# Performance work log

Measured on AMD Instinct MI355X. Metric: run time of the kernel, lower is better.

The kernel has to match this reference:

```python
import jax, jax.numpy as jnp
import numpy as np

B, S, HID = 1, 2048, 2048
H, KH, D = 16, 8, 128          # query heads, kv heads, head_dim
GROUPS = H // KH                # num_key_value_groups = 2
EPS = 1e-6
SCALE = D ** -0.5
NEG = -1e9


def rmsnorm(x, w):
    # torch.nn.RMSNorm over last dim with learned weight
    return x * jax.lax.rsqrt(jnp.mean(x * x, axis=-1, keepdims=True) + EPS) * w


def rope(x, cos, sin):
    # x: [b, s, h, d]; cos/sin: [s, d//2]  (rotate-half style, matching apply_rotary_emb_single)
    half = x.shape[-1] // 2
    xr, xi = x[..., :half], x[..., half:]
    c = cos[None, :, None, :]
    s = sin[None, :, None, :]
    return jnp.concatenate([xr * c - xi * s, xr * s + xi * c], axis=-1)


def setup_inputs() -> dict:
    key = jax.random.key(0)
    ks = jax.random.split(key, 8)
    hidden_states = jax.random.normal(ks[0], (B, S, HID), jnp.float32)
    # real RoPE angle tables (theta=1e6, Qwen3-style), shape [S, D//2]
    inv_freq = 1.0 / (1e6 ** (np.arange(0, D, 2, dtype=np.float32) / D))
    ang = np.arange(S, dtype=np.float32)[:, None] * inv_freq[None, :]
    freqs_cos = jnp.asarray(np.cos(ang), jnp.float32)
    freqs_sin = jnp.asarray(np.sin(ang), jnp.float32)
    # additive causal mask [1, S, S]
    causal = jnp.tril(jnp.ones((S, S), jnp.bool_))
    atten_mask = jnp.where(causal, 0.0, NEG).astype(jnp.float32)[None]
    # learned params (no bias: attention_bias=False)
    Wq = jax.random.normal(ks[1], (H * D, HID), jnp.float32) * 0.02
    Wk = jax.random.normal(ks[2], (KH * D, HID), jnp.float32) * 0.02
    Wv = jax.random.normal(ks[3], (KH * D, HID), jnp.float32) * 0.02
    Wo = jax.random.normal(ks[4], (HID, H * D), jnp.float32) * 0.02
    q_norm_w = 1.0 + 0.01 * jax.random.normal(ks[5], (D,), jnp.float32)
    k_norm_w = 1.0 + 0.01 * jax.random.normal(ks[6], (D,), jnp.float32)
    return {"hidden_states": hidden_states, "freqs_cos": freqs_cos, "freqs_sin": freqs_sin,
            "atten_mask": atten_mask, "Wq": Wq, "Wk": Wk, "Wv": Wv, "Wo": Wo,
            "q_norm_w": q_norm_w, "k_norm_w": k_norm_w}


def reference(hidden_states, freqs_cos, freqs_sin, atten_mask, Wq, Wk, Wv, Wo, q_norm_w, k_norm_w):
    b, s, _ = hidden_states.shape
    q = (hidden_states @ Wq.T).reshape(b, s, H, D)
    k = (hidden_states @ Wk.T).reshape(b, s, KH, D)
    v = (hidden_states @ Wv.T).reshape(b, s, KH, D)
    q = rope(rmsnorm(q, q_norm_w), freqs_cos, freqs_sin)
    k = rope(rmsnorm(k, k_norm_w), freqs_cos, freqs_sin)
    # GQA: head i uses kv head i // GROUPS -> repeat kv heads in-order
    k_exp = jnp.repeat(k, GROUPS, axis=2)  # [b, s, H, d]
    v_exp = jnp.repeat(v, GROUPS, axis=2)
    scores = jnp.einsum('bshd,bthd->bhst', q, k_exp) * SCALE + atten_mask[:, None, :, :]
    attn = jax.nn.softmax(scores, axis=-1)
    y = jnp.einsum('bhst,bthd->bshd', attn, v_exp).reshape(b, s, H * D)
    y = y @ Wo.T
    # output_new_cache_only: last-position k (post-norm/RoPE) and raw v per kv head
    k_new = jnp.transpose(k[:, -1], (1, 0, 2))  # [KH, b, D]
    v_new = jnp.transpose(v[:, -1], (1, 0, 2))  # [KH, b, D]
    return y, k_new, v_new
```

## Files before the change

### kernel.cpp

```cpp
#include <hip/hip_runtime.h>
#include <hip/hip_bf16.h>
#include <math.h>

#define S_LEN 2048
#define HID 2048
#define NH 16
#define NKH 8
#define HD 128
#define QKV_N 4096
#define SCALE 0.08838834764831845f
#define EPS 1e-6f
#define LOG2E 1.4426950408889634f
#define QSCALE (SCALE * LOG2E)

typedef __hip_bfloat16 bf16;
typedef unsigned int u32;
typedef __bf16 bf16x8 __attribute__((ext_vector_type(8)));
typedef float f32x4 __attribute__((ext_vector_type(4)));

#define MFMA(a, b, c) __builtin_amdgcn_mfma_f32_16x16x32_bf16(a, b, c, 0, 0, 0)

static __device__ __forceinline__ bf16x8 ld_frag(const bf16* p) {
    return __builtin_bit_cast(bf16x8, *(const uint4*)p);
}

static __device__ __forceinline__ void gload_lds16(const void* g, void* l) {
    __builtin_amdgcn_global_load_lds(
        (const __attribute__((address_space(1))) u32*)g,
        (__attribute__((address_space(3))) u32*)l, 16, 0, 0);
}

__global__ __launch_bounds__(256) void cvt5(
    const float* __restrict__ s0, const float* __restrict__ s1,
    const float* __restrict__ s2, const float* __restrict__ s3,
    const float* __restrict__ s4,
    bf16* __restrict__ d0, bf16* __restrict__ d1, bf16* __restrict__ d2,
    bf16* __restrict__ d3, bf16* __restrict__ d4)
{
    int i = blockIdx.x * 256 + threadIdx.x;
    const float* s; bf16* d; int off;
    if (i < (1 << 20))                   { s = s0; d = d0; off = 0; }
    else if (i < (2 << 20))              { s = s1; d = d1; off = 1 << 20; }
    else if (i < (2 << 20) + (1 << 19))  { s = s2; d = d2; off = 2 << 20; }
    else if (i < (3 << 20))              { s = s3; d = d3; off = (2 << 20) + (1 << 19); }
    else                                 { s = s4; d = d4; off = 3 << 20; }
    int j = i - off;
    float4 v = ((const float4*)s)[j];
    union { ushort4 u; bf16 h[4]; } o;
    o.h[0] = __float2bfloat16(v.x);
    o.h[1] = __float2bfloat16(v.y);
    o.h[2] = __float2bfloat16(v.z);
    o.h[3] = __float2bfloat16(v.w);
    *(ushort4*)(d + 4 * (size_t)j) = o.u;
}

__global__ __launch_bounds__(256, 2) void gemm_qkv(
    const bf16* __restrict__ A, const bf16* __restrict__ B,
    bf16* __restrict__ qkvb, bf16* __restrict__ vT,
    const float* __restrict__ fcos, const float* __restrict__ fsin,
    const float* __restrict__ qw, const float* __restrict__ kw,
    float* __restrict__ knew, float* __restrict__ vnew)
{
    __shared__ bf16 As[2][128 * 64];
    __shared__ bf16 Bs[2][128 * 64];
    __shared__ float red[2][2][64];
    const int tid = threadIdx.x;
    const int n0 = blockIdx.x * 128, m0 = blockIdx.y * 128;
    const int w = tid >> 6, lane = tid & 63;
    const int l15 = lane & 15, quad = lane >> 4;
    const int wr = (w >> 1) * 64;
    const int wcg = (w & 1) * 32;

    f32x4 acc[4][4];
    #pragma unroll
    for (int i = 0; i < 4; ++i)
        #pragma unroll
        for (int j = 0; j < 4; ++j)
            acc[i][j] = f32x4{0.f, 0.f, 0.f, 0.f};

    const int srow8 = lane >> 3;
    const int sls = ((lane & 7) ^ srow8) * 8;

    auto stage = [&](int k0, int nb) {
        #pragma unroll
        for (int j = 0; j < 8; ++j) {
            int c = 8 * w + j;
            if (c < 16) {
                int row = c * 8 + srow8;
                gload_lds16(A + (size_t)(m0 + row) * HID + k0 + sls, &As[nb][c * 512]);
            } else {
                int row = (c - 16) * 8 + srow8;
                gload_lds16(B + (size_t)(n0 + row) * HID + k0 + sls, &Bs[nb][(c - 16) * 512]);
            }
        }
    };

    stage(0, 0);
    for (int kt = 0; kt < HID / 64; ++kt) {
        const int pp = kt & 1;
        __syncthreads();
        if (kt + 1 < HID / 64) stage((kt + 1) * 64, pp ^ 1);

        #pragma unroll
        for (int kc = 0; kc < 2; ++kc) {
            const int ph = ((kc * 4 + quad) ^ (l15 & 7)) * 8;
            bf16x8 av[4], bv[4];
            #pragma unroll
            for (int i = 0; i < 4; ++i)
                av[i] = ld_frag(&As[pp][(wr + i * 16 + l15) * 64 + ph]);
            #pragma unroll
            for (int j = 0; j < 4; ++j)
                bv[j] = ld_frag(&Bs[pp][(wcg + (j & 1) * 16 + (j >> 1) * 64 + l15) * 64 + ph]);
            #pragma unroll
            for (int i = 0; i < 4; ++i)
                #pragma unroll
                for (int j = 0; j < 4; ++j)
                    acc[i][j] = MFMA(av[i], bv[j], acc[i][j]);
        }
    }

    const int hblk = n0 >> 7;
    if (hblk < 24) {
        float ssq[4][4];
        #pragma unroll
        for (int i = 0; i < 4; ++i)
            #pragma unroll
            for (int rr = 0; rr < 4; ++rr) {
                float ss = 0.f;
                #pragma unroll
                for (int j = 0; j < 4; ++j) ss += acc[i][j][rr] * acc[i][j][rr];
                ss += __shfl_xor(ss, 1);
                ss += __shfl_xor(ss, 2);
                ss += __shfl_xor(ss, 4);
                ss += __shfl_xor(ss, 8);
                ssq[i][rr] = ss;
                if (l15 == 0)
                    red[w >> 1][w & 1][i * 16 + quad * 4 + rr] = ss;
            }
        __syncthreads();

        const float* wgt = (hblk < 16) ? qw : kw;
        float wv[4];
        #pragma unroll
        for (int j = 0; j < 4; ++j)
            wv[j] = wgt[wcg + (j & 1) * 16 + (j >> 1) * 64 + l15];
        const size_t cb = (hblk < 16) ? (size_t)hblk * HD
                                      : (size_t)HID + (size_t)(hblk - 16) * HD;

        #pragma unroll
        for (int i = 0; i < 4; ++i)
            #pragma unroll
            for (int rr = 0; rr < 4; ++rr) {
                int rloc = i * 16 + quad * 4 + rr;
                int srow = m0 + wr + rloc;
                float tot = ssq[i][rr] + red[w >> 1][(w & 1) ^ 1][rloc];
                float rrn = rsqrtf(tot * (1.0f / 128.0f) + EPS);
                float x[4], res[4];
                #pragma unroll
                for (int j = 0; j < 4; ++j) x[j] = acc[i][j][rr] * rrn * wv[j];
                #pragma unroll
                for (int j2 = 0; j2 < 2; ++j2) {
                    float c = fcos[srow * 64 + wcg + j2 * 16 + l15];
                    float s = fsin[srow * 64 + wcg + j2 * 16 + l15];
                    res[j2]     = x[j2] * c - x[j2 + 2] * s;
                    res[j2 + 2] = x[j2] * s + x[j2 + 2] * c;
                }
                if (hblk < 16) {
                    #pragma unroll
                    for (int j = 0; j < 4; ++j)
                        qkvb[(size_t)srow * QKV_N + cb + wcg + (j & 1) * 16 +
                             (j >> 1) * 64 + l15] = __float2bfloat16(res[j] * QSCALE);
                } else {
                    #pragma unroll
                    for (int j = 0; j < 4; ++j)
                        qkvb[(size_t)srow * QKV_N + cb + wcg + (j & 1) * 16 +
                             (j >> 1) * 64 + l15] = __float2bfloat16(res[j]);
                    if (srow == S_LEN - 1) {
                        #pragma unroll
                        for (int j = 0; j < 4; ++j)
                            knew[(hblk - 16) * HD + wcg + (j & 1) * 16 +
                                 (j >> 1) * 64 + l15] = res[j];
                    }
                }
            }
    } else {
        const int kh = hblk - 24;
        #pragma unroll
        for (int i = 0; i < 4; ++i) {
            int rowbase = m0 + wr + i * 16 + quad * 4;
            #pragma unroll
            for (int j = 0; j < 4; ++j) {
                int d = wcg + (j & 1) * 16 + (j >> 1) * 64 + l15;
                union { uint2 u; bf16 hh[4]; } pk;
                #pragma unroll
                for (int r = 0; r < 4; ++r)
                    pk.hh[r] = __float2bfloat16(acc[i][j][r]);
                *(uint2*)&vT[(size_t)(kh * HD + d) * S_LEN + rowbase] = pk.u;
                if (rowbase == S_LEN - 4)
                    vnew[kh * HD + d] = acc[i][j][3];
            }
        }
    }
}

__global__ __launch_bounds__(256, 2) void gemm_n64(
    const bf16* __restrict__ A, const bf16* __restrict__ B,
    float* __restrict__ C, int M, int N, int K)
{
    __shared__ bf16 As[2][128 * 64];
    __shared__ bf16 Bs[2][64 * 64];
    const int tid = threadIdx.x;
    const int n0 = blockIdx.x * 64, m0 = blockIdx.y * 128;
    const int w = tid >> 6, lane = tid & 63;
    const int l15 = lane & 15, quad = lane >> 4;

    f32x4 acc[2][4];
    #pragma unroll
    for (int i = 0; i < 2; ++i)
        #pragma unroll
        for (int j = 0; j < 4; ++j)
            acc[i][j] = f32x4{0.f, 0.f, 0.f, 0.f};

    const int srow8 = lane >> 3;
    const int sls = ((lane & 7) ^ srow8) * 8;

    auto stage = [&](int k0, int nb) {
        #pragma unroll
        for (int j = 0; j < 6; ++j) {
            int c = 6 * w + j;
            if (c < 16) {
                int row = c * 8 + srow8;
                gload_lds16(A + (size_t)(m0 + row) * K + k0 + sls, &As[nb][c * 512]);
            } else {
                int row = (c - 16) * 8 + srow8;
                gload_lds16(B + (size_t)(n0 + row) * K + k0 + sls, &Bs[nb][(c - 16) * 512]);
            }
        }
    };

    stage(0, 0);
    for (int kt = 0; kt < K / 64; ++kt) {
        const int pp = kt & 1;
        __syncthreads();
        if (kt + 1 < K / 64) stage((kt + 1) * 64, pp ^ 1);

        #pragma unroll
        for (int kc = 0; kc < 2; ++kc) {
            const int ph = ((kc * 4 + quad) ^ (l15 & 7)) * 8;
            bf16x8 av[2], bv[4];
            av[0] = ld_frag(&As[pp][(w * 32 + l15) * 64 + ph]);
            av[1] = ld_frag(&As[pp][(w * 32 + 16 + l15) * 64 + ph]);
            #pragma unroll
            for (int j = 0; j < 4; ++j)
                bv[j] = ld_frag(&Bs[pp][(j * 16 + l15) * 64 + ph]);
            #pragma unroll
            for (int i = 0; i < 2; ++i)
                #pragma unroll
                for (int j = 0; j < 4; ++j)
                    acc[i][j] = MFMA(av[i], bv[j], acc[i][j]);
        }
    }

    #pragma unroll
    for (int i = 0; i < 2; ++i)
        #pragma unroll
        for (int j = 0; j < 4; ++j)
            #pragma unroll
            for (int r = 0; r < 4; ++r)
                C[(size_t)(m0 + w * 32 + i * 16 + quad * 4 + r) * N +
                  n0 + j * 16 + l15] = acc[i][j][r];
}

__global__ __launch_bounds__(256, 2) void attn_mfma(
    const bf16* __restrict__ qkvb, const bf16* __restrict__ vT,
    bf16* __restrict__ outb)
{
    __shared__ bf16 Ks[2][64 * 128];
    __shared__ bf16 Vs[2][128 * 64];
    __shared__ bf16 Ps[4][16 * 72];
    __shared__ float lred[4][4][16];

    const int x = blockIdx.x;
    const int h = blockIdx.y, kvh = h >> 1;
    int a = (x & 1) ? (31 - (x >> 1)) : (x >> 1);
    const int qb = (h < 8) ? a : 31 - a;
    const int tid = threadIdx.x, w = tid >> 6, lane = tid & 63;
    const int l15 = lane & 15, quad = lane >> 4;

    bf16x8 qf[4][4];
    #pragma unroll
    for (int j = 0; j < 4; ++j)
        #pragma unroll
        for (int dk = 0; dk < 4; ++dk)
            qf[j][dk] = ld_frag(qkvb + (size_t)(qb * 64 + j * 16 + l15) * QKV_N +
                                h * HD + dk * 32 + quad * 8);

    f32x4 o[8];
    #pragma unroll
    for (int dt = 0; dt < 8; ++dt) o[dt] = f32x4{0.f, 0.f, 0.f, 0.f};
    float l_st[4] = {0.f, 0.f, 0.f, 0.f};

    auto stage = [&](int t, int nb) {
        const int kt0 = t * 64;
        if (w < 2) {
            #pragma unroll
            for (int c = 0; c < 8; ++c) {
                int chunk = w * 8 + c;
                int row = 4 * chunk + (lane >> 4);
                int ls = (lane & 15) ^ (row & 15);
                gload_lds16(qkvb + (size_t)(kt0 + row) * QKV_N + HID +
                            kvh * HD + ls * 8,
                            &Ks[nb][chunk * 512]);
            }
        } else {
            #pragma unroll
            for (int c = 0; c < 8; ++c) {
                int chunk = (w - 2) * 8 + c;
                int row = 8 * chunk + (lane >> 3);
                int ls = (lane & 7) ^ ((lane >> 3) & 7);
                gload_lds16(vT + (size_t)(kvh * HD + row) * S_LEN + kt0 + ls * 8,
                            &Vs[nb][chunk * 512]);
            }
        }
    };

    stage(0, 0);
    for (int t = 0; t <= qb; ++t) {
        const int pp = t & 1;
        __syncthreads();
        if (t < qb) stage(t + 1, pp ^ 1);

        f32x4 sc[4];
        #pragma unroll
        for (int j = 0; j < 4; ++j) sc[j] = f32x4{0.f, 0.f, 0.f, 0.f};
        #pragma unroll
        for (int dk = 0; dk < 4; ++dk) {
            bf16x8 kf = ld_frag(&Ks[pp][(w * 16 + l15) * 128 +
                                        (((dk * 4 + quad) ^ l15) & 15) * 8]);
            #pragma unroll
            for (int j = 0; j < 4; ++j)
                sc[j] = MFMA(kf, qf[j][dk], sc[j]);
        }

        if (t == qb) {
            #pragma unroll
            for (int j = 0; j < 4; ++j)
                #pragma unroll
                for (int r = 0; r < 4; ++r)
                    if (w * 16 + quad * 4 + r > j * 16 + l15) sc[j][r] = -1e30f;
        }

        #pragma unroll
        for (int j = 0; j < 4; ++j) {
            union { uint2 u; bf16 hh[4]; } pk;
            #pragma unroll
            for (int r = 0; r < 4; ++r) {
                float p = exp2f(sc[j][r]);
                pk.hh[r] = __float2bfloat16(p);
                l_st[j] += p;
            }
            *(uint2*)&Ps[j][l15 * 72 + w * 16 + quad * 4] = pk.u;
        }

        asm volatile("s_waitcnt lgkmcnt(0)" ::: "memory");
        __builtin_amdgcn_s_barrier();

        #pragma unroll
        for (int kc = 0; kc < 2; ++kc) {
            bf16x8 pf[4];
            #pragma unroll
            for (int j = 0; j < 4; ++j)
                pf[j] = ld_frag(&Ps[j][l15 * 72 + kc * 32 + quad * 8]);
            #pragma unroll
            for (int dt = 0; dt < 2; ++dt) {
                bf16x8 vf = ld_frag(&Vs[pp][((w * 2 + dt) * 16 + l15) * 64 +
                                            (((kc * 4 + quad) ^ (l15 & 7)) * 8)]);
                #pragma unroll
                for (int j = 0; j < 4; ++j)
                    o[dt * 4 + j] = MFMA(vf, pf[j], o[dt * 4 + j]);
            }
        }
    }

    #pragma unroll
    for (int j = 0; j < 4; ++j) {
        l_st[j] += __shfl_xor(l_st[j], 16, 64);
        l_st[j] += __shfl_xor(l_st[j], 32, 64);
    }
    if (lane < 16) {
        #pragma unroll
        for (int j = 0; j < 4; ++j) lred[w][j][lane] = l_st[j];
    }
    __syncthreads();
    #pragma unroll
    for (int j = 0; j < 4; ++j) {
        float inv = 1.0f / (lred[0][j][l15] + lred[1][j][l15] +
                            lred[2][j][l15] + lred[3][j][l15]);
        int qg = qb * 64 + j * 16 + l15;
        #pragma unroll
        for (int dt = 0; dt < 2; ++dt) {
            union { uint2 u; bf16 hh[4]; } pk;
            #pragma unroll
            for (int r = 0; r < 4; ++r)
                pk.hh[r] = __float2bfloat16(o[dt * 4 + j][r] * inv);
            *(uint2*)&outb[(size_t)qg * HID + h * HD + w * 32 + dt * 16 + quad * 4] = pk.u;
        }
    }
}

extern "C" void kernel_launch(void* const* d_in, const int* in_sizes, int n_in,
                              void* d_out, int out_size, void* d_ws, size_t ws_size,
                              hipStream_t stream) {
    const float* hidden = (const float*)d_in[0];
    const float* fcos   = (const float*)d_in[1];
    const float* fsin   = (const float*)d_in[2];
    const float* Wq = (const float*)d_in[4];
    const float* Wk = (const float*)d_in[5];
    const float* Wv = (const float*)d_in[6];
    const float* Wo = (const float*)d_in[7];
    const float* qw = (const float*)d_in[8];
    const float* kw = (const float*)d_in[9];
    float* out = (float*)d_out;

    bf16* qkvb  = (bf16*)d_ws;
    bf16* vT    = qkvb + (size_t)S_LEN * QKV_N;
    bf16* attnb = vT + (size_t)NKH * HD * S_LEN;
    bf16* wqkvb = attnb + (size_t)S_LEN * HID;
    bf16* hidb  = wqkvb + (size_t)QKV_N * HID;
    bf16* wob   = hidb + (size_t)S_LEN * HID;

    float* knew = out + (size_t)S_LEN * HID;
    float* vnew = knew + NKH * HD;

    cvt5<<<16384, 256, 0, stream>>>(
        hidden, Wq, Wk, Wv, Wo,
        hidb, wqkvb, wqkvb + (size_t)HID * HID,
        wqkvb + (size_t)(HID + NKH * HD) * HID, wob);

    gemm_qkv<<<dim3(QKV_N / 128, S_LEN / 128), 256, 0, stream>>>(
        hidb, wqkvb, qkvb, vT, fcos, fsin, qw, kw, knew, vnew);

    attn_mfma<<<dim3(32, NH), 256, 0, stream>>>(qkvb, vT, attnb);

    gemm_n64<<<dim3(HID / 64, S_LEN / 128), 256, 0, stream>>>(
        attnb, wob, out, S_LEN, HID, HID);
}
```

Before: 240.6 us.

## Fuse fp32-to-bf16 conversion into GEMM operand staging, drop separate convert kernel

Removes the standalone conversion kernel that turned hidden states and all weights into bf16 in workspace. The QKV and output-projection GEMMs now load fp32 operands into registers, convert them to bf16 and write them to LDS, software-pipelined one tile ahead. This drops a full read/write pass over the inputs and weights and one launch. In exchange the GEMMs move twice the bytes per tile from global/L2 and use more registers in place of direct global-to-LDS loads.

```diff
diff --git a/kernel.cpp b/kernel.cpp
--- a/kernel.cpp
+++ b/kernel.cpp
@@ -30,32 +30,20 @@
         (__attribute__((address_space(3))) u32*)l, 16, 0, 0);
 }
 
-__global__ __launch_bounds__(256) void cvt5(
-    const float* __restrict__ s0, const float* __restrict__ s1,
-    const float* __restrict__ s2, const float* __restrict__ s3,
-    const float* __restrict__ s4,
-    bf16* __restrict__ d0, bf16* __restrict__ d1, bf16* __restrict__ d2,
-    bf16* __restrict__ d3, bf16* __restrict__ d4)
-{
-    int i = blockIdx.x * 256 + threadIdx.x;
-    const float* s; bf16* d; int off;
-    if (i < (1 << 20))                   { s = s0; d = d0; off = 0; }
-    else if (i < (2 << 20))              { s = s1; d = d1; off = 1 << 20; }
-    else if (i < (2 << 20) + (1 << 19))  { s = s2; d = d2; off = 2 << 20; }
-    else if (i < (3 << 20))              { s = s3; d = d3; off = (2 << 20) + (1 << 19); }
-    else                                 { s = s4; d = d4; off = 3 << 20; }
-    int j = i - off;
-    float4 v = ((const float4*)s)[j];
-    union { ushort4 u; bf16 h[4]; } o;
-    o.h[0] = __float2bfloat16(v.x);
-    o.h[1] = __float2bfloat16(v.y);
-    o.h[2] = __float2bfloat16(v.z);
-    o.h[3] = __float2bfloat16(v.w);
-    *(ushort4*)(d + 4 * (size_t)j) = o.u;
+static __device__ __forceinline__ uint4 cvt8(float4 lo, float4 hi) {
+    union { uint4 u; bf16 h[8]; } pk;
+    pk.h[0] = __float2bfloat16(lo.x); pk.h[1] = __float2bfloat16(lo.y);
+    pk.h[2] = __float2bfloat16(lo.z); pk.h[3] = __float2bfloat16(lo.w);
+    pk.h[4] = __float2bfloat16(hi.x); pk.h[5] = __float2bfloat16(hi.y);
+    pk.h[6] = __float2bfloat16(hi.z); pk.h[7] = __float2bfloat16(hi.w);
+    return pk.u;
 }
 
 __global__ __launch_bounds__(256, 2) void gemm_qkv(
-    const bf16* __restrict__ A, const bf16* __restrict__ B,
+    const float* __restrict__ A,
+    const float* __restrict__ Wq,
+    const float* __restrict__ Wk,
+    const float* __restrict__ Wv,
     bf16* __restrict__ qkvb, bf16* __restrict__ vT,
     const float* __restrict__ fcos, const float* __restrict__ fsin,
     const float* __restrict__ qw, const float* __restrict__ kw,
@@ -71,6 +59,12 @@
     const int wr = (w >> 1) * 64;
     const int wcg = (w & 1) * 32;
 
+    const int hblk = n0 >> 7;
+    const float* Bsrc; int brow0;
+    if (hblk < 16)      { Bsrc = Wq; brow0 = n0; }
+    else if (hblk < 24) { Bsrc = Wk; brow0 = n0 - 2048; }
+    else                { Bsrc = Wv; brow0 = n0 - 3072; }
+
     f32x4 acc[4][4];
     #pragma unroll
     for (int i = 0; i < 4; ++i)
@@ -81,25 +75,36 @@
     const int srow8 = lane >> 3;
     const int sls = ((lane & 7) ^ srow8) * 8;
 
-    auto stage = [&](int k0, int nb) {
+    float4 rlo[8], rhi[8];
+
+    auto issue = [&](int k0) {
         #pragma unroll
         for (int j = 0; j < 8; ++j) {
             int c = 8 * w + j;
-            if (c < 16) {
-                int row = c * 8 + srow8;
-                gload_lds16(A + (size_t)(m0 + row) * HID + k0 + sls, &As[nb][c * 512]);
-            } else {
-                int row = (c - 16) * 8 + srow8;
-                gload_lds16(B + (size_t)(n0 + row) * HID + k0 + sls, &Bs[nb][(c - 16) * 512]);
-            }
-        }
-    };
-
-    stage(0, 0);
+            const float* src = (c < 16)
+                ? A    + (size_t)(m0 + c * 8 + srow8) * HID + k0 + sls
+                : Bsrc + (size_t)(brow0 + (c - 16) * 8 + srow8) * HID + k0 + sls;
+            rlo[j] = *(const float4*)src;
+            rhi[j] = *(const float4*)(src + 4);
+        }
+    };
+    auto writeb = [&](int nb) {
+        #pragma unroll
+        for (int j = 0; j < 8; ++j) {
+            int c = 8 * w + j;
+            uint4 u = cvt8(rlo[j], rhi[j]);
+            bf16* dst = (c < 16)
+                ? &As[nb][c * 512 + srow8 * 64 + (lane & 7) * 8]
+                : &Bs[nb][(c - 16) * 512 + srow8 * 64 + (lane & 7) * 8];
+            *(uint4*)dst = u;
+        }
+    };
+
+    issue(0);  writeb(0);
+    issue(64);
     for (int kt = 0; kt < HID / 64; ++kt) {
         const int pp = kt & 1;
         __syncthreads();
-        if (kt + 1 < HID / 64) stage((kt + 1) * 64, pp ^ 1);
 
         #pragma unroll
         for (int kc = 0; kc < 2; ++kc) {
@@ -117,9 +122,13 @@
                 for (int j = 0; j < 4; ++j)
                     acc[i][j] = MFMA(av[i], bv[j], acc[i][j]);
         }
-    }
-
-    const int hblk = n0 >> 7;
+
+        if (kt + 1 < HID / 64) {
+            writeb(pp ^ 1);
+            if (kt + 2 < HID / 64) issue((kt + 2) * 64);
+        }
+    }
+
     if (hblk < 24) {
         float ssq[4][4];
         #pragma unroll
@@ -204,7 +213,7 @@
 }
 
 __global__ __launch_bounds__(256, 2) void gemm_n64(
-    const bf16* __restrict__ A, const bf16* __restrict__ B,
+    const bf16* __restrict__ A, const float* __restrict__ Bw,
     float* __restrict__ C, int M, int N, int K)
 {
     __shared__ bf16 As[2][128 * 64];
@@ -224,25 +233,38 @@
     const int srow8 = lane >> 3;
     const int sls = ((lane & 7) ^ srow8) * 8;
 
-    auto stage = [&](int k0, int nb) {
-        #pragma unroll
-        for (int j = 0; j < 6; ++j) {
-            int c = 6 * w + j;
-            if (c < 16) {
-                int row = c * 8 + srow8;
-                gload_lds16(A + (size_t)(m0 + row) * K + k0 + sls, &As[nb][c * 512]);
-            } else {
-                int row = (c - 16) * 8 + srow8;
-                gload_lds16(B + (size_t)(n0 + row) * K + k0 + sls, &Bs[nb][(c - 16) * 512]);
-            }
-        }
-    };
-
-    stage(0, 0);
+    auto stageA = [&](int k0, int nb) {
+        #pragma unroll
+        for (int j = 0; j < 4; ++j) {
+            int c = 4 * w + j;
+            gload_lds16(A + (size_t)(m0 + c * 8 + srow8) * K + k0 + sls,
+                        &As[nb][c * 512]);
+        }
+    };
+    float4 blo[2], bhi[2];
+    auto issueB = [&](int k0) {
+        #pragma unroll
+        for (int j = 0; j < 2; ++j) {
+            const float* src = Bw + (size_t)(n0 + (2 * w + j) * 8 + srow8) * K + k0 + sls;
+            blo[j] = *(const float4*)src;
+            bhi[j] = *(const float4*)(src + 4);
+        }
+    };
+    auto writeB = [&](int nb) {
+        #pragma unroll
+        for (int j = 0; j < 2; ++j) {
+            uint4 u = cvt8(blo[j], bhi[j]);
+            *(uint4*)&Bs[nb][(2 * w + j) * 512 + srow8 * 64 + (lane & 7) * 8] = u;
+        }
+    };
+
+    issueB(0);  writeB(0);
+    stageA(0, 0);
+    issueB(64);
     for (int kt = 0; kt < K / 64; ++kt) {
         const int pp = kt & 1;
         __syncthreads();
-        if (kt + 1 < K / 64) stage((kt + 1) * 64, pp ^ 1);
+        if (kt + 1 < K / 64) stageA((kt + 1) * 64, pp ^ 1);
 
         #pragma unroll
         for (int kc = 0; kc < 2; ++kc) {
@@ -258,6 +280,11 @@
                 #pragma unroll
                 for (int j = 0; j < 4; ++j)
                     acc[i][j] = MFMA(av[i], bv[j], acc[i][j]);
+        }
+
+        if (kt + 1 < K / 64) {
+            writeB(pp ^ 1);
+            if (kt + 2 < K / 64) issueB((kt + 2) * 64);
         }
     }
 
@@ -425,23 +452,15 @@
     bf16* qkvb  = (bf16*)d_ws;
     bf16* vT    = qkvb + (size_t)S_LEN * QKV_N;
     bf16* attnb = vT + (size_t)NKH * HD * S_LEN;
-    bf16* wqkvb = attnb + (size_t)S_LEN * HID;
-    bf16* hidb  = wqkvb + (size_t)QKV_N * HID;
-    bf16* wob   = hidb + (size_t)S_LEN * HID;
 
     float* knew = out + (size_t)S_LEN * HID;
     float* vnew = knew + NKH * HD;
 
-    cvt5<<<16384, 256, 0, stream>>>(
-        hidden, Wq, Wk, Wv, Wo,
-        hidb, wqkvb, wqkvb + (size_t)HID * HID,
-        wqkvb + (size_t)(HID + NKH * HD) * HID, wob);
-
     gemm_qkv<<<dim3(QKV_N / 128, S_LEN / 128), 256, 0, stream>>>(
-        hidb, wqkvb, qkvb, vT, fcos, fsin, qw, kw, knew, vnew);
+        hidden, Wq, Wk, Wv, qkvb, vT, fcos, fsin, qw, kw, knew, vnew);
 
     attn_mfma<<<dim3(32, NH), 256, 0, stream>>>(qkvb, vT, attnb);
 
     gemm_n64<<<dim3(HID / 64, S_LEN / 128), 256, 0, stream>>>(
-        attnb, wob, out, S_LEN, HID, HID);
-}
+        attnb, Wo, out, S_LEN, HID, HID);
+}
```

After: 264.7 us. 1.1x slower.

## Share K/V tiles across both GQA query heads in one 512-thread block

Applied to the files above, without the earlier changes.

The attention kernel now launches one block per KV head and query tile, with 8 waves: two groups of four, each group handling one of the two query heads that share the KV head. K and V tiles are staged once into LDS and reused by both heads, halving global K/V traffic and staging work per head. In exchange the grid shrinks from 512 to 256 blocks, each block is larger with launch bounds of one block per SM, and the per-head P buffers and row-sum reductions are duplicated in shared memory. Fewer, larger blocks may reduce occupancy and make load balancing coarser across the causal tiles.

```diff
diff --git a/kernel.cpp b/kernel.cpp
--- a/kernel.cpp
+++ b/kernel.cpp
@@ -271,20 +271,23 @@
                   n0 + j * 16 + l15] = acc[i][j][r];
 }
 
-__global__ __launch_bounds__(256, 2) void attn_mfma(
+__global__ __launch_bounds__(512, 1) void attn_mfma(
     const bf16* __restrict__ qkvb, const bf16* __restrict__ vT,
     bf16* __restrict__ outb)
 {
     __shared__ bf16 Ks[2][64 * 128];
     __shared__ bf16 Vs[2][128 * 64];
-    __shared__ bf16 Ps[4][16 * 72];
-    __shared__ float lred[4][4][16];
+    __shared__ bf16 Ps[8][16 * 72];
+    __shared__ float lred[2][4][4][16];
 
     const int x = blockIdx.x;
-    const int h = blockIdx.y, kvh = h >> 1;
+    const int kvh = blockIdx.y;
     int a = (x & 1) ? (31 - (x >> 1)) : (x >> 1);
-    const int qb = (h < 8) ? a : 31 - a;
-    const int tid = threadIdx.x, w = tid >> 6, lane = tid & 63;
+    const int qb = (kvh & 1) ? 31 - a : a;
+    const int tid = threadIdx.x;
+    const int w8 = tid >> 6, lane = tid & 63;
+    const int g = w8 >> 2, w = w8 & 3;
+    const int h = kvh * 2 + g;
     const int l15 = lane & 15, quad = lane >> 4;
 
     bf16x8 qf[4][4];
@@ -302,24 +305,21 @@
 
     auto stage = [&](int t, int nb) {
         const int kt0 = t * 64;
-        if (w < 2) {
-            #pragma unroll
-            for (int c = 0; c < 8; ++c) {
-                int chunk = w * 8 + c;
-                int row = 4 * chunk + (lane >> 4);
+        #pragma unroll
+        for (int j = 0; j < 4; ++j) {
+            int c = w8 * 4 + j;
+            if (c < 16) {
+                int row = 4 * c + (lane >> 4);
                 int ls = (lane & 15) ^ (row & 15);
                 gload_lds16(qkvb + (size_t)(kt0 + row) * QKV_N + HID +
                             kvh * HD + ls * 8,
-                            &Ks[nb][chunk * 512]);
-            }
-        } else {
-            #pragma unroll
-            for (int c = 0; c < 8; ++c) {
-                int chunk = (w - 2) * 8 + c;
-                int row = 8 * chunk + (lane >> 3);
+                            &Ks[nb][c * 512]);
+            } else {
+                int cv = c - 16;
+                int row = 8 * cv + (lane >> 3);
                 int ls = (lane & 7) ^ ((lane >> 3) & 7);
                 gload_lds16(vT + (size_t)(kvh * HD + row) * S_LEN + kt0 + ls * 8,
-                            &Vs[nb][chunk * 512]);
+                            &Vs[nb][cv * 512]);
             }
         }
     };
@@ -359,7 +359,7 @@
                 pk.hh[r] = __float2bfloat16(p);
                 l_st[j] += p;
             }
-            *(uint2*)&Ps[j][l15 * 72 + w * 16 + quad * 4] = pk.u;
+            *(uint2*)&Ps[g * 4 + j][l15 * 72 + w * 16 + quad * 4] = pk.u;
         }
 
         asm volatile("s_waitcnt lgkmcnt(0)" ::: "memory");
@@ -370,7 +370,7 @@
             bf16x8 pf[4];
             #pragma unroll
             for (int j = 0; j < 4; ++j)
-                pf[j] = ld_frag(&Ps[j][l15 * 72 + kc * 32 + quad * 8]);
+                pf[j] = ld_frag(&Ps[g * 4 + j][l15 * 72 + kc * 32 + quad * 8]);
             #pragma unroll
             for (int dt = 0; dt < 2; ++dt) {
                 bf16x8 vf = ld_frag(&Vs[pp][((w * 2 + dt) * 16 + l15) * 64 +
@@ -389,13 +389,13 @@
     }
     if (lane < 16) {
         #pragma unroll
-        for (int j = 0; j < 4; ++j) lred[w][j][lane] = l_st[j];
+        for (int j = 0; j < 4; ++j) lred[g][w][j][lane] = l_st[j];
     }
     __syncthreads();
     #pragma unroll
     for (int j = 0; j < 4; ++j) {
-        float inv = 1.0f / (lred[0][j][l15] + lred[1][j][l15] +
-                            lred[2][j][l15] + lred[3][j][l15]);
+        float inv = 1.0f / (lred[g][0][j][l15] + lred[g][1][j][l15] +
+                            lred[g][2][j][l15] + lred[g][3][j][l15]);
         int qg = qb * 64 + j * 16 + l15;
         #pragma unroll
         for (int dt = 0; dt < 2; ++dt) {
@@ -440,7 +440,7 @@
     gemm_qkv<<<dim3(QKV_N / 128, S_LEN / 128), 256, 0, stream>>>(
         hidb, wqkvb, qkvb, vT, fcos, fsin, qw, kw, knew, vnew);
 
-    attn_mfma<<<dim3(32, NH), 256, 0, stream>>>(qkvb, vT, attnb);
+    attn_mfma<<<dim3(32, NKH), 512, 0, stream>>>(qkvb, vT, attnb);
 
     gemm_n64<<<dim3(HID / 64, S_LEN / 128), 256, 0, stream>>>(
         attnb, wob, out, S_LEN, HID, HID);
```

After: 250.5 us. 1.04x slower.
